# Optimization experiments

Hardware: AMD Instinct MI355X
Metric: run time of the kernel (lower is better)

## Reference

```python
import jax, jax.numpy as jnp
import numpy as np

KERNEL_SIZE = 4  # W


def setup_inputs() -> dict:
    key = jax.random.key(0)
    k1, k2, k3, k4 = jax.random.split(key, 4)
    B, T, D, H, W = 2, 4096, 2048, 2048, KERNEL_SIZE
    x = jax.random.normal(k1, (B, T, D), dtype=jnp.float32)
    # torch nn.Linear weight layout: [out_features, in_features]
    w1 = jax.random.normal(k2, (H, D), dtype=jnp.float32) * 0.02
    w2_w = jax.random.normal(k3, (D * W, H), dtype=jnp.float32) * 0.02
    w2_b = jax.random.normal(k4, (D * W,), dtype=jnp.float32) * 0.02
    return {"x": x, "w1": w1, "w2_w": w2_w, "w2_b": w2_b}


def reference(x, w1, w2_w, w2_b):
    # x: [B, T, D]
    B, T, D = x.shape
    W = KERNEL_SIZE
    # kernel generator MLP: Linear(D->H, no bias) -> silu -> Linear(H->D*W, bias)
    h = jax.nn.silu(jnp.einsum('btd,hd->bth', x, w1))
    flat_kernels = jnp.einsum('bth,kh->btk', h, w2_w) + w2_b
    # rearrange 'b t (d w) -> b t d w' (d major, w minor)
    kernels = flat_kernels.reshape(B, T, D, W)
    # causal windows: pad W-1 on the left of time, gather W shifted views
    x_pad = jnp.pad(x, ((0, 0), (W - 1, 0), (0, 0)))
    windows = jnp.stack([x_pad[:, w:w + T, :] for w in range(W)], axis=-1)  # [B,T,D,W]
    out = jnp.sum(windows * kernels, axis=-1)  # per-token dynamic depthwise causal conv
    return jax.nn.silu(out)  # self.activation == 'silu'
```

## Files before the change

### kernel.cpp

```cpp
#include <hip/hip_runtime.h>
#include <hip/hip_bf16.h>
#include <math.h>

#define B_DIM 2
#define T_DIM 4096
#define D_DIM 2048
#define H_DIM 2048
#define W_K   4
#define M_DIM (B_DIM * T_DIM)
#define N2_DIM (D_DIM * W_K)

typedef __bf16 bf16x8 __attribute__((ext_vector_type(8)));
typedef float  f32x4  __attribute__((ext_vector_type(4)));

#define BM 256
#define BN 256
#define BKT 64
#define XW_STRIDE 68

__device__ __forceinline__ unsigned short f2bf(float f) {
    unsigned int u = __float_as_uint(f);
    unsigned int r = (u + 0x7FFFu + ((u >> 16) & 1u)) >> 16;
    return (unsigned short)r;
}

__device__ __forceinline__ float silu_f(float v) {
    return v / (1.0f + __expf(-v));
}

__global__ void cvt_f32_to_bf16(const float* __restrict__ in,
                                unsigned short* __restrict__ out, int n4) {
    int i = blockIdx.x * blockDim.x + threadIdx.x;
    if (i >= n4) return;
    float4 v = reinterpret_cast<const float4*>(in)[i];
    ushort4 o;
    o.x = f2bf(v.x); o.y = f2bf(v.y); o.z = f2bf(v.z); o.w = f2bf(v.w);
    reinterpret_cast<ushort4*>(out)[i] = o;
}

__device__ __forceinline__ bf16x8 lds_frag(const unsigned short* buf, int r, int kb) {
    int lin = r * 128 + (kb ^ ((r & 7) << 4));
    return *reinterpret_cast<const bf16x8*>(reinterpret_cast<const char*>(buf) + lin);
}

#define BARRIER()    __builtin_amdgcn_s_barrier()
#define WAIT_VM(N)   asm volatile("s_waitcnt vmcnt(" #N ")" ::: "memory")

#define STAGE64(basePtr, soffX, ko, dstUshort, chunk) \
    __builtin_amdgcn_global_load_lds( \
        (const __attribute__((address_space(1))) void*)((basePtr) + (soffX) + (size_t)(chunk) * 64 * K + (ko)), \
        (__attribute__((address_space(3))) void*)(reinterpret_cast<char*>(dstUshort) + ((chunk) << 13) + (wave << 10)), \
        16, 0, 0)

#define MG_MFMA(mg, AF) \
    _Pragma("unroll") for (int kk = 0; kk < 2; ++kk) \
    _Pragma("unroll") for (int mrel = 0; mrel < 2; ++mrel) \
    _Pragma("unroll") for (int nf = 0; nf < 4; ++nf) \
        acc[(mg)*2 + mrel][nf] = __builtin_amdgcn_mfma_f32_16x16x32_bf16( \
            AF[mrel][kk], bfrag[nf][kk], acc[(mg)*2 + mrel][nf], 0, 0, 0)

#define READ_B(tB) \
    _Pragma("unroll") for (int nf = 0; nf < 4; ++nf) \
    _Pragma("unroll") for (int kk = 0; kk < 2; ++kk) \
        bfrag[nf][kk] = lds_frag(tB, wc*64 + nf*16 + ln15, kk*64 + kb16)

#define READ_A(AF, tA, mg) \
    _Pragma("unroll") for (int mrel = 0; mrel < 2; ++mrel) \
    _Pragma("unroll") for (int kk = 0; kk < 2; ++kk) \
        AF[mrel][kk] = lds_frag(tA, wr*128 + (mg)*32 + mrel*16 + ln15, kk*64 + kb16)

#define KTILE_R(bi, jj, SA2, SB, VMN) do { \
    const unsigned short* tA = smem + (bi) * 16384; \
    const unsigned short* tB = smem + 32768 + (bi) * 16384; \
    unsigned short* oA = smem + ((bi) ^ 1) * 16384; \
    unsigned short* cA = smem + (bi) * 16384; \
    unsigned short* cB = smem + 32768 + (bi) * 16384; \
    READ_B(tB); \
    READ_A(af0, tA, 0); \
    if (SA2) { const int ko = ((jj) + 1) << 6; \
        STAGE64(baseA, soffA, ko, oA, 1); STAGE64(baseA, soffA, ko, oA, 3); } \
    READ_A(af1, tA, 1); \
    __builtin_amdgcn_s_setprio(1); MG_MFMA(0, af0); __builtin_amdgcn_s_setprio(0); \
    __builtin_amdgcn_s_setprio(1); MG_MFMA(1, af1); __builtin_amdgcn_s_setprio(0); \
    BARRIER(); \
    READ_A(af0, tA, 2); \
    if (SB) { const int ko = ((jj) + 2) << 6; \
        STAGE64(baseB, soffB, ko, cB, 0); STAGE64(baseB, soffB, ko, cB, 1); \
        STAGE64(baseA, soffA, ko, cA, 0); STAGE64(baseA, soffA, ko, cA, 2); } \
    READ_A(af1, tA, 3); \
    __builtin_amdgcn_s_setprio(1); MG_MFMA(2, af0); __builtin_amdgcn_s_setprio(0); \
    if (SB) { const int ko = ((jj) + 2) << 6; \
        STAGE64(baseB, soffB, ko, cB, 2); STAGE64(baseB, soffB, ko, cB, 3); } \
    __builtin_amdgcn_s_setprio(1); MG_MFMA(3, af1); __builtin_amdgcn_s_setprio(0); \
    WAIT_VM(VMN); \
    BARRIER(); \
} while (0)

template <int EPI>
__global__ __launch_bounds__(512, 2)
void gemm8p(const unsigned short* __restrict__ A,
            const unsigned short* __restrict__ Bm,
            int M, int N, int K,
            unsigned short* __restrict__ Hout,
            const float* __restrict__ bias,
            const float* __restrict__ Xf,
            float* __restrict__ Out) {
    __shared__ __align__(16) unsigned short smem[65536];

    const int tid  = threadIdx.x;
    const int wave = tid >> 6, lane = tid & 63;
    const int wr = wave >> 2, wc = wave & 3;
    const int ln15 = lane & 15;
    const int kb16 = (lane >> 4) * 16;

    const int GX = gridDim.x, GY = gridDim.y;
    const int bid = blockIdx.y * GX + blockIdx.x;
    const int xcd = bid & 7;
    const int idx = bid >> 3;
    const int W_ = GX >> 2;
    const int rr = idx / W_, cc = idx % W_;
    const int by = (xcd >> 2) * (GY >> 1) + rr;
    const int bx = (xcd & 3) * W_ + cc;
    const int m0 = by * BM, n0 = bx * BN;

    const int nk = K >> 6;

    const int srow = (wave << 3) + (lane >> 3);
    const int scol = (((lane & 7) ^ (lane >> 3)) << 3);
    const size_t soffA = (size_t)srow * K + scol;
    const int prow = ((srow & 15) << 2) | (srow >> 4);
    const size_t soffB = (size_t)prow * K + scol;
    const unsigned short* baseA = A + (size_t)m0 * K;
    const unsigned short* baseB = Bm + (size_t)n0 * K;

    f32x4 acc[8][4];
#pragma unroll
    for (int i = 0; i < 8; ++i)
#pragma unroll
        for (int j = 0; j < 4; ++j) acc[i][j] = (f32x4)0.0f;

    bf16x8 bfrag[4][2], af0[2][2], af1[2][2];

    {
        unsigned short* dA0 = smem;
        unsigned short* dB0 = smem + 32768;
        unsigned short* dA1 = smem + 16384;
        unsigned short* dB1 = smem + 49152;
        STAGE64(baseB, soffB, 0, dB0, 0); STAGE64(baseB, soffB, 0, dB0, 1);
        STAGE64(baseB, soffB, 0, dB0, 2); STAGE64(baseB, soffB, 0, dB0, 3);
        STAGE64(baseA, soffA, 0, dA0, 0); STAGE64(baseA, soffA, 0, dA0, 1);
        STAGE64(baseA, soffA, 0, dA0, 2); STAGE64(baseA, soffA, 0, dA0, 3);
        STAGE64(baseB, soffB, BKT, dB1, 0); STAGE64(baseB, soffB, BKT, dB1, 1);
        STAGE64(baseA, soffA, BKT, dA1, 0); STAGE64(baseA, soffA, BKT, dA1, 2);
        STAGE64(baseB, soffB, BKT, dB1, 2); STAGE64(baseB, soffB, BKT, dB1, 3);
    }
    WAIT_VM(6);
    BARRIER();

    for (int it = 0; it < (nk >> 1) - 1; ++it) {
        const int j = it << 1;
        KTILE_R(0, j,     1, 1, 6);
        KTILE_R(1, j + 1, 1, 1, 6);
    }
    KTILE_R(0, nk - 2, 1, 0, 0);
    KTILE_R(1, nk - 1, 0, 0, 0);

    if (EPI == 0) {
        const size_t colbase = n0 + wc * 64 + ln15 * 4;
#pragma unroll
        for (int mf = 0; mf < 8; ++mf) {
            int rowb = m0 + wr * 128 + mf * 16 + (lane >> 4) * 4;
#pragma unroll
            for (int r2 = 0; r2 < 4; ++r2) {
                ushort4 h4;
                h4.x = f2bf(silu_f(acc[mf][0][r2]));
                h4.y = f2bf(silu_f(acc[mf][1][r2]));
                h4.z = f2bf(silu_f(acc[mf][2][r2]));
                h4.w = f2bf(silu_f(acc[mf][3][r2]));
                *reinterpret_cast<ushort4*>(&Hout[(size_t)(rowb + r2) * N + colbase]) = h4;
            }
        }
    } else {
        const int t0 = m0 & (T_DIM - 1);
        const int bidx = m0 >> 12;
        const int dbase = n0 >> 2;
        float* Xw = reinterpret_cast<float*>(smem);
        for (int idx2 = tid; idx2 < 259 * 16; idx2 += 512) {
            int rw = idx2 >> 4, q = (idx2 & 15) << 2;
            int ts = t0 - 3 + rw;
            float4 v = make_float4(0.f, 0.f, 0.f, 0.f);
            if (ts >= 0)
                v = *reinterpret_cast<const float4*>(
                    &Xf[((size_t)bidx * T_DIM + ts) * D_DIM + dbase + q]);
            float* p = &Xw[rw * XW_STRIDE + q];
            p[0] = v.x; p[1] = v.y; p[2] = v.z; p[3] = v.w;
        }
        __syncthreads();

        const int dloc = wc * 16 + ln15;
        const float4 bias4 = *reinterpret_cast<const float4*>(
            &bias[n0 + wc * 64 + ln15 * 4]);
#pragma unroll
        for (int mf = 0; mf < 8; ++mf) {
            int lrow0 = wr * 128 + mf * 16 + (lane >> 4) * 4;
            float xr[7];
#pragma unroll
            for (int q = 0; q < 7; ++q)
                xr[q] = Xw[(lrow0 + q) * XW_STRIDE + dloc];
#pragma unroll
            for (int r2 = 0; r2 < 4; ++r2) {
                float v = (acc[mf][0][r2] + bias4.x) * xr[r2 + 0];
                v      += (acc[mf][1][r2] + bias4.y) * xr[r2 + 1];
                v      += (acc[mf][2][r2] + bias4.z) * xr[r2 + 2];
                v      += (acc[mf][3][r2] + bias4.w) * xr[r2 + 3];
                int lrow = lrow0 + r2;
                Out[((size_t)bidx * T_DIM + (t0 + lrow)) * D_DIM + dbase + dloc] = silu_f(v);
            }
        }
    }
}

extern "C" void kernel_launch(void* const* d_in, const int* in_sizes, int n_in,
                              void* d_out, int out_size, void* d_ws, size_t ws_size,
                              hipStream_t stream) {
    const float* x    = (const float*)d_in[0];
    const float* w1   = (const float*)d_in[1];
    const float* w2w  = (const float*)d_in[2];
    const float* w2b  = (const float*)d_in[3];
    float* out = (float*)d_out;

    unsigned short* ws0 = (unsigned short*)d_ws;
    unsigned short* ws1 = ws0 + (size_t)M_DIM * D_DIM;
    unsigned short* ws2 = ws1 + (size_t)H_DIM * D_DIM;

    const int CT = 256;
    {
        int n4 = (M_DIM * D_DIM) / 4;
        cvt_f32_to_bf16<<<(n4 + CT - 1) / CT, CT, 0, stream>>>(x, ws0, n4);
    }
    {
        int n4 = (H_DIM * D_DIM) / 4;
        cvt_f32_to_bf16<<<(n4 + CT - 1) / CT, CT, 0, stream>>>(w1, ws1, n4);
    }
    gemm8p<0><<<dim3(H_DIM / BN, M_DIM / BM), 512, 0, stream>>>(
        ws0, ws1, M_DIM, H_DIM, D_DIM, ws2, nullptr, nullptr, nullptr);
    {
        int n4 = (N2_DIM * H_DIM) / 4;
        cvt_f32_to_bf16<<<(n4 + CT - 1) / CT, CT, 0, stream>>>(w2w, ws0, n4);
    }
    gemm8p<1><<<dim3(N2_DIM / BN, M_DIM / BM), 512, 0, stream>>>(
        ws2, ws0, M_DIM, N2_DIM, H_DIM, nullptr, w2b, x, out);
}
```

Baseline: 339.6 us.

## Restructure GEMM K-loop to single-barrier double buffering with deferred last MFMA group

Replaces the two-barrier-per-tile pipeline, which prefetched two tiles ahead with split staging, with a one-barrier-per-tile double buffer. The next tile is fully staged into the other buffer while the current one is read, and the fourth MFMA group is deferred into the next iteration, after the barrier, to overlap with its LDS reads. The aim is fewer barriers and better interleaving of MFMA with loads. In exchange prefetch depth drops to one tile and it waits for all outstanding loads each iteration, which may expose global memory latency; it also adds fragment registers and an extra sync before the epilogue reuses LDS.

Result: faster. 330.6 us (-2.7%).

```diff
diff --git a/kernel.cpp b/kernel.cpp
--- a/kernel.cpp
+++ b/kernel.cpp
@@ -69,30 +69,28 @@
     _Pragma("unroll") for (int kk = 0; kk < 2; ++kk) \
         AF[mrel][kk] = lds_frag(tA, wr*128 + (mg)*32 + mrel*16 + ln15, kk*64 + kb16)
 
-#define KTILE_R(bi, jj, SA2, SB, VMN) do { \
+#define KTILE_S(bi, jj, PREV, SG) do { \
     const unsigned short* tA = smem + (bi) * 16384; \
     const unsigned short* tB = smem + 32768 + (bi) * 16384; \
-    unsigned short* oA = smem + ((bi) ^ 1) * 16384; \
-    unsigned short* cA = smem + (bi) * 16384; \
-    unsigned short* cB = smem + 32768 + (bi) * 16384; \
+    unsigned short* dA = smem + ((bi) ^ 1) * 16384; \
+    unsigned short* dB = smem + 32768 + ((bi) ^ 1) * 16384; \
+    if (PREV) { __builtin_amdgcn_s_setprio(1); MG_MFMA(3, afD); __builtin_amdgcn_s_setprio(0); } \
     READ_B(tB); \
+    if (SG) { const int ko = ((jj) + 1) << 6; \
+        STAGE64(baseB, soffB, ko, dB, 0); STAGE64(baseB, soffB, ko, dB, 1); \
+        STAGE64(baseB, soffB, ko, dB, 2); STAGE64(baseB, soffB, ko, dB, 3); } \
     READ_A(af0, tA, 0); \
-    if (SA2) { const int ko = ((jj) + 1) << 6; \
-        STAGE64(baseA, soffA, ko, oA, 1); STAGE64(baseA, soffA, ko, oA, 3); } \
     READ_A(af1, tA, 1); \
+    if (SG) { const int ko = ((jj) + 1) << 6; \
+        STAGE64(baseA, soffA, ko, dA, 0); STAGE64(baseA, soffA, ko, dA, 1); \
+        STAGE64(baseA, soffA, ko, dA, 2); STAGE64(baseA, soffA, ko, dA, 3); } \
     __builtin_amdgcn_s_setprio(1); MG_MFMA(0, af0); __builtin_amdgcn_s_setprio(0); \
+    READ_A(af0, tA, 2); \
     __builtin_amdgcn_s_setprio(1); MG_MFMA(1, af1); __builtin_amdgcn_s_setprio(0); \
-    BARRIER(); \
-    READ_A(af0, tA, 2); \
-    if (SB) { const int ko = ((jj) + 2) << 6; \
-        STAGE64(baseB, soffB, ko, cB, 0); STAGE64(baseB, soffB, ko, cB, 1); \
-        STAGE64(baseA, soffA, ko, cA, 0); STAGE64(baseA, soffA, ko, cA, 2); } \
-    READ_A(af1, tA, 3); \
+    READ_A(afD, tA, 3); \
     __builtin_amdgcn_s_setprio(1); MG_MFMA(2, af0); __builtin_amdgcn_s_setprio(0); \
-    if (SB) { const int ko = ((jj) + 2) << 6; \
-        STAGE64(baseB, soffB, ko, cB, 2); STAGE64(baseB, soffB, ko, cB, 3); } \
-    __builtin_amdgcn_s_setprio(1); MG_MFMA(3, af1); __builtin_amdgcn_s_setprio(0); \
-    WAIT_VM(VMN); \
+     \
+    WAIT_VM(0); \
     BARRIER(); \
 } while (0)
 
@@ -139,31 +137,27 @@
 #pragma unroll
         for (int j = 0; j < 4; ++j) acc[i][j] = (f32x4)0.0f;
 
-    bf16x8 bfrag[4][2], af0[2][2], af1[2][2];
+    bf16x8 bfrag[4][2], af0[2][2], af1[2][2], afD[2][2];
 
     {
         unsigned short* dA0 = smem;
         unsigned short* dB0 = smem + 32768;
-        unsigned short* dA1 = smem + 16384;
-        unsigned short* dB1 = smem + 49152;
         STAGE64(baseB, soffB, 0, dB0, 0); STAGE64(baseB, soffB, 0, dB0, 1);
         STAGE64(baseB, soffB, 0, dB0, 2); STAGE64(baseB, soffB, 0, dB0, 3);
         STAGE64(baseA, soffA, 0, dA0, 0); STAGE64(baseA, soffA, 0, dA0, 1);
         STAGE64(baseA, soffA, 0, dA0, 2); STAGE64(baseA, soffA, 0, dA0, 3);
-        STAGE64(baseB, soffB, BKT, dB1, 0); STAGE64(baseB, soffB, BKT, dB1, 1);
-        STAGE64(baseA, soffA, BKT, dA1, 0); STAGE64(baseA, soffA, BKT, dA1, 2);
-        STAGE64(baseB, soffB, BKT, dB1, 2); STAGE64(baseB, soffB, BKT, dB1, 3);
-    }
-    WAIT_VM(6);
+    }
+    WAIT_VM(0);
     BARRIER();
 
-    for (int it = 0; it < (nk >> 1) - 1; ++it) {
-        const int j = it << 1;
-        KTILE_R(0, j,     1, 1, 6);
-        KTILE_R(1, j + 1, 1, 1, 6);
-    }
-    KTILE_R(0, nk - 2, 1, 0, 0);
-    KTILE_R(1, nk - 1, 0, 0, 0);
+    KTILE_S(0, 0, 0, 1);
+    for (int it = 0; it < (nk - 2) / 2; ++it) {
+        const int j = 1 + (it << 1);
+        KTILE_S(1, j,     1, 1);
+        KTILE_S(0, j + 1, 1, 1);
+    }
+    KTILE_S(1, nk - 1, 1, 0);
+    __builtin_amdgcn_s_setprio(1); MG_MFMA(3, afD); __builtin_amdgcn_s_setprio(0);
 
     if (EPI == 0) {
         const size_t colbase = n0 + wc * 64 + ln15 * 4;
@@ -185,6 +179,7 @@
         const int bidx = m0 >> 12;
         const int dbase = n0 >> 2;
         float* Xw = reinterpret_cast<float*>(smem);
+        __syncthreads();
         for (int idx2 = tid; idx2 < 259 * 16; idx2 += 512) {
             int rw = idx2 >> 4, q = (idx2 & 15) << 2;
             int ts = t0 - 3 + rw;
```
